# Optimization experiments

Hardware: AMD Instinct MI355X
Metric: run time of the kernel (lower is better)

## Reference

```python
import jax, jax.numpy as jnp
import numpy as np

EPS = 1e-8

def _normalize(x, eps=EPS):
    mean = jnp.mean(x, axis=-1, keepdims=True)
    var = jnp.var(x, axis=-1, keepdims=True)  # unbiased=False
    return (x - mean) / jnp.sqrt(var + eps)


def setup_inputs() -> dict:
    key = jax.random.key(0)
    ks = jax.random.split(key, 10)
    B, M, d = 8, 50000, 256
    out_units, num_heads, gsl_hidden = 256, 8, 16
    s = 0.02
    return {
        "h": jax.random.normal(ks[0], (B, M, d), dtype=jnp.float32),
        "att_w": jax.random.normal(ks[1], (d, num_heads), dtype=jnp.float32) * s,
        "att_b": jnp.zeros((num_heads,), dtype=jnp.float32),
        "w_w": jax.random.normal(ks[2], (d, out_units), dtype=jnp.float32) * s,
        "res_w": jax.random.normal(ks[3], (d, out_units), dtype=jnp.float32) * s,
        "res_b": jnp.zeros((out_units,), dtype=jnp.float32),
        "gsl1_w": jax.random.normal(ks[4], (d, gsl_hidden), dtype=jnp.float32) * s,
        "gsl1_b": jnp.zeros((gsl_hidden,), dtype=jnp.float32),
        "gsl2_w": jax.random.normal(ks[5], (gsl_hidden, 1), dtype=jnp.float32) * s,
        "gsl2_b": jnp.zeros((1,), dtype=jnp.float32),
        "k": 500,
    }


def reference(h, att_w, att_b, w_w, res_w, res_b, gsl1_w, gsl1_b, gsl2_w, gsl2_b, k):
    B, M, d = h.shape
    num_heads = att_w.shape[1]
    out_units = w_w.shape[1]
    head_dim = out_units // num_heads

    # additive attention scores per head: [B, M, H]
    A = jax.nn.relu(jnp.einsum('bmd,dh->bmh', h, att_w) + att_b)
    # value projection: [B, M, out]
    H_lin = jnp.einsum('bmd,de->bme', h, w_w)

    # learned graph-structure-learning scores: [B, M]
    S_hidden = jax.nn.relu(jnp.einsum('bmd,dg->bmg', h, gsl1_w) + gsl1_b)
    S = jax.nn.sigmoid(jnp.einsum('bmg,go->bmo', S_hidden, gsl2_w) + gsl2_b)[..., 0]

    # top-k mask over nodes (dim=1)
    k_eff = min(k, M)
    topk_vals, _ = jax.lax.top_k(S, k_eff)  # sorted descending
    kth = topk_vals[:, -1:]                 # [B, 1]
    mask = (S >= kth).astype(h.dtype)       # [B, M]

    # masked scores (zeros at masked positions, NOT -inf: faithful to source)
    A_mod = A * mask[:, :, None]            # [B, M, H]
    weights = jax.nn.softmax(A_mod, axis=1)  # softmax over M per head
    # (dropout is a no-op in eval mode)

    # per-head weighted sum over nodes, then concat heads along feature dim
    Hr = H_lin.reshape(B, M, num_heads, head_dim)
    out = jnp.einsum('bmh,bmhd->bhd', weights, Hr).reshape(B, 1, out_units)

    # residual from mean-pooled input
    Q_res = jax.nn.relu(jnp.einsum('bmd,de->bme', jnp.mean(h, axis=1, keepdims=True), res_w) + res_b)
    out = jax.nn.relu(out + Q_res)
    return _normalize(out), mask[:, None, :]
```

## Files before the change

kernel.cpp:

```cpp
#include <hip/hip_runtime.h>
#include <cstdint>
#include <cstddef>


#define MM     50000
#define BATCH  8
#define TILES  196
#define CH     8
#define NCHUNK 32

#define OFF_A        0u
#define OFF_KEYS     12800000u
#define OFF_SUMH     16000000u
#define OFF_UCORR    16016384u
#define OFF_ZCORR    16147456u
#define OFF_CCNT     16147968u
#define ZERO_SZ      148000u
#define OFF_KTH      16148000u
#define OFF_COMPACT  16148064u

__global__ __launch_bounds__(256) void k1_main(
    const float* __restrict__ h,
    const float* __restrict__ att_w,
    const float* __restrict__ att_b,
    const float* __restrict__ g1w,
    const float* __restrict__ g1b,
    const float* __restrict__ g2w,
    const float* __restrict__ g2b,
    float* __restrict__ Aout,
    unsigned long long* __restrict__ keys,
    double* __restrict__ sumh)
{
    __shared__ double gw_s[256][16];
    __shared__ float  aw_s[256][8];
    __shared__ float  tile[4][CH][65];
    __shared__ float  lsum[256];

    const int tid  = threadIdx.x;
    const int w    = tid >> 6;
    const int lane = tid & 63;

    for (int i = tid; i < 4096; i += 256) gw_s[i >> 4][i & 15] = (double)g1w[i];
    for (int i = tid; i < 2048; i += 256) aw_s[i >> 3][i & 7]  = att_w[i];
    lsum[tid] = 0.0f;
    __syncthreads();

    const int bid = blockIdx.x;
    const int b   = bid / TILES;
    const int t0  = bid % TILES;
    const int wave_row0 = t0 * 256 + w * 64;
    const size_t bbase = (size_t)b * MM;

    const int kq   = lane & 1;
    const int rsub = lane >> 1;

    float  aacc[8];
    double gacc[16];
#pragma unroll
    for (int j = 0; j < 8; ++j) aacc[j] = 0.0f;
#pragma unroll
    for (int g = 0; g < 16; ++g) gacc[g] = 0.0;

    const int m0 = wave_row0 + rsub;
    const int m1 = wave_row0 + 32 + rsub;
    const size_t r0c = bbase + (size_t)((m0 < MM) ? m0 : (MM - 1));
    const size_t r1c = bbase + (size_t)((m1 < MM) ? m1 : (MM - 1));

    {
        float4 v0 = *(const float4*)(h + r0c * 256 + kq * 4);
        float4 v1 = *(const float4*)(h + r1c * 256 + kq * 4);
        if (m0 >= MM) { v0.x = v0.y = v0.z = v0.w = 0.f; }
        if (m1 >= MM) { v1.x = v1.y = v1.z = v1.w = 0.f; }
        tile[w][kq*4+0][rsub] = v0.x;  tile[w][kq*4+1][rsub] = v0.y;
        tile[w][kq*4+2][rsub] = v0.z;  tile[w][kq*4+3][rsub] = v0.w;
        tile[w][kq*4+0][32+rsub] = v1.x;  tile[w][kq*4+1][32+rsub] = v1.y;
        tile[w][kq*4+2][32+rsub] = v1.z;  tile[w][kq*4+3][32+rsub] = v1.w;
    }

    for (int c = 0; c < NCHUNK; ++c) {
        float4 n0, n1;
        const bool has = (c + 1 < NCHUNK);
        if (has) {
            const int kof = (c + 1) * CH + kq * 4;
            n0 = *(const float4*)(h + r0c * 256 + kof);
            n1 = *(const float4*)(h + r1c * 256 + kof);
            if (m0 >= MM) { n0.x = n0.y = n0.z = n0.w = 0.f; }
            if (m1 >= MM) { n1.x = n1.y = n1.z = n1.w = 0.f; }
        }
        const int k0 = c * CH;
#pragma unroll
        for (int kk = 0; kk < CH; ++kk) {
            float  hv = tile[w][kk][lane];
            double hd = (double)hv;
            const int kx = k0 + kk;
#pragma unroll
            for (int j = 0; j < 8; ++j) aacc[j] = fmaf(hv, aw_s[kx][j], aacc[j]);
#pragma unroll
            for (int g = 0; g < 16; ++g) gacc[g] = fma(hd, gw_s[kx][g], gacc[g]);
        }
        {
            const int dsub = lane & 7;
            const int rq   = lane >> 3;
            float s = 0.f;
#pragma unroll
            for (int i = 0; i < 8; ++i) s += tile[w][dsub][rq * 8 + i];
            s += __shfl_xor(s, 8, 64);
            s += __shfl_xor(s, 16, 64);
            s += __shfl_xor(s, 32, 64);
            if (lane < 8) atomicAdd(&lsum[k0 + lane], s);
        }
        if (has) {
            tile[w][kq*4+0][rsub] = n0.x;  tile[w][kq*4+1][rsub] = n0.y;
            tile[w][kq*4+2][rsub] = n0.z;  tile[w][kq*4+3][rsub] = n0.w;
            tile[w][kq*4+0][32+rsub] = n1.x;  tile[w][kq*4+1][32+rsub] = n1.y;
            tile[w][kq*4+2][32+rsub] = n1.z;  tile[w][kq*4+3][32+rsub] = n1.w;
        }
    }

    const int m = wave_row0 + lane;
    if (m < MM) {
        size_t row = bbase + (size_t)m;
        float4 A0, A1;
        A0.x = fmaxf(aacc[0] + att_b[0], 0.f);
        A0.y = fmaxf(aacc[1] + att_b[1], 0.f);
        A0.z = fmaxf(aacc[2] + att_b[2], 0.f);
        A0.w = fmaxf(aacc[3] + att_b[3], 0.f);
        A1.x = fmaxf(aacc[4] + att_b[4], 0.f);
        A1.y = fmaxf(aacc[5] + att_b[5], 0.f);
        A1.z = fmaxf(aacc[6] + att_b[6], 0.f);
        A1.w = fmaxf(aacc[7] + att_b[7], 0.f);
        float4* Ap = (float4*)(Aout + row * 8);
        Ap[0] = A0; Ap[1] = A1;

        double z = (double)g2b[0];
#pragma unroll
        for (int g = 0; g < 16; ++g) {
            double sg = gacc[g] + (double)g1b[g];
            sg = sg > 0.0 ? sg : 0.0;
            z = fma(sg, (double)g2w[g], z);
        }
        long long uz = __double_as_longlong(z);
        unsigned long long key = (uz < 0)
            ? ~((unsigned long long)uz)
            : ((unsigned long long)uz | 0x8000000000000000ULL);
        keys[row] = key;
    }
    __syncthreads();
    atomicAdd(&sumh[b * 256 + tid], (double)lsum[tid]);
}

__global__ __launch_bounds__(1024) void k2_select(
    const unsigned long long* __restrict__ keys,
    const int* __restrict__ kptr,
    unsigned long long* __restrict__ kth)
{
    __shared__ unsigned long long buf[4096];
    __shared__ int s_cnt;
    __shared__ unsigned long long s_pivot;

    const int b    = blockIdx.x;
    const int tid  = threadIdx.x;
    const int lane = tid & 63;
    const size_t base = (size_t)b * MM;
    const int kval = min(*kptr, MM);

    buf[tid] = keys[base + (size_t)tid * 48];
    __syncthreads();
    for (int sz = 2; sz <= 1024; sz <<= 1)
        for (int j = sz >> 1; j > 0; j >>= 1) {
            __syncthreads();
            int i = tid, ixj = i ^ j;
            if (ixj > i) {
                unsigned long long a = buf[i], c = buf[ixj];
                bool up = ((i & sz) == 0);
                if ((up && a > c) || (!up && a < c)) { buf[i] = c; buf[ixj] = a; }
            }
        }
    __syncthreads();

    int R = 40;
    unsigned long long pivot = 0;
    for (int iter = 0; iter < 24; ++iter) {
        if (tid == 0) { s_pivot = buf[1023 - R]; s_cnt = 0; }
        __syncthreads();
        pivot = s_pivot;
        int loc = 0;
        for (int m = tid; m < MM; m += 1024)
            loc += (keys[base + m] >= pivot) ? 1 : 0;
        loc += __shfl_xor(loc, 32, 64);
        loc += __shfl_xor(loc, 16, 64);
        loc += __shfl_xor(loc, 8, 64);
        loc += __shfl_xor(loc, 4, 64);
        loc += __shfl_xor(loc, 2, 64);
        loc += __shfl_xor(loc, 1, 64);
        if (lane == 0) atomicAdd(&s_cnt, loc);
        __syncthreads();
        int n_ge = s_cnt;
        if (n_ge >= kval && n_ge <= 4096) break;
        R = (n_ge < kval) ? min(R + 48, 1023) : max(R - 16, 0);
        __syncthreads();
    }

    if (tid == 0) s_cnt = 0;
    __syncthreads();
    for (int m = tid; m < MM; m += 1024) {
        unsigned long long x = keys[base + m];
        bool p = (x >= pivot);
        unsigned long long ball = __ballot(p);
        int wbase = 0;
        if (lane == 0) { int wc = __popcll(ball); if (wc) wbase = atomicAdd(&s_cnt, wc); }
        wbase = __shfl(wbase, 0, 64);
        if (p) {
            int pos = wbase + __popcll(ball & ((1ull << lane) - 1ull));
            if (pos < 4096) buf[pos] = x;
        }
    }
    __syncthreads();
    const int n = min(s_cnt, 4096);

    unsigned long long p64 = 0;
    int kk = kval;
    for (int bit = 63; bit >= 0; --bit) {
        if (tid == 0) s_cnt = 0;
        __syncthreads();
        unsigned long long himask = (bit == 63) ? 0ull : (~0ull << (bit + 1));
        int loc = 0;
        for (int i = tid; i < n; i += 1024) {
            unsigned long long x = buf[i];
            if (((x ^ p64) & himask) == 0ull && ((x >> bit) & 1ull)) loc++;
        }
        loc += __shfl_xor(loc, 32, 64);
        loc += __shfl_xor(loc, 16, 64);
        loc += __shfl_xor(loc, 8, 64);
        loc += __shfl_xor(loc, 4, 64);
        loc += __shfl_xor(loc, 2, 64);
        loc += __shfl_xor(loc, 1, 64);
        if (lane == 0 && loc) atomicAdd(&s_cnt, loc);
        __syncthreads();
        int c1 = s_cnt;
        if (c1 >= kk) p64 |= (1ull << bit); else kk -= c1;
        __syncthreads();
    }
    if (tid == 0) kth[b] = p64;
}

__global__ __launch_bounds__(256) void k3_mask(
    const unsigned long long* __restrict__ keys,
    const unsigned long long* __restrict__ kth,
    float* __restrict__ maskout,
    int* __restrict__ ccnt,
    int* __restrict__ compact)
{
    int bid = blockIdx.x;
    int b = bid / TILES, t0 = bid % TILES;
    int m = t0 * 256 + threadIdx.x;
    int lane = threadIdx.x & 63;
    bool mk = false;
    if (m < MM) {
        size_t row = (size_t)b * MM + m;
        mk = (keys[row] >= kth[b]);
        maskout[row] = mk ? 1.0f : 0.0f;
    }
    unsigned long long ball = __ballot(mk);
    int wbase = 0;
    if (lane == 0) { int wc = __popcll(ball); if (wc) wbase = atomicAdd(&ccnt[b], wc); }
    wbase = __shfl(wbase, 0, 64);
    if (mk) {
        int pos = wbase + __popcll(ball & ((1ull << lane) - 1ull));
        if (pos < 2048) compact[b * 2048 + pos] = m;
    }
}

__global__ __launch_bounds__(256) void k4_corr(
    const float* __restrict__ h,
    const float* __restrict__ A,
    const int* __restrict__ compact,
    const int* __restrict__ ccnt,
    double* __restrict__ Ucorr,
    double* __restrict__ Zcorr)
{
    int b    = blockIdx.x >> 5;
    int part = blockIdx.x & 31;
    int tid  = threadIdx.x;
    int n = min(ccnt[b], 2048);
    float acc[8], zac[8];
#pragma unroll
    for (int j = 0; j < 8; ++j) { acc[j] = 0.f; zac[j] = 0.f; }
    for (int i = part; i < n; i += 32) {
        int m = compact[b * 2048 + i];
        size_t row = (size_t)b * MM + m;
        const float* Ap = A + row * 8;
        float hv = h[row * 256 + tid];
#pragma unroll
        for (int j = 0; j < 8; ++j) {
            float ex = expf(Ap[j]) - 1.0f;
            acc[j] = fmaf(ex, hv, acc[j]);
            zac[j] += ex;
        }
    }
#pragma unroll
    for (int j = 0; j < 8; ++j)
        atomicAdd(&Ucorr[(b * 8 + j) * 256 + tid], (double)acc[j]);
    if (tid == 0) {
#pragma unroll
        for (int j = 0; j < 8; ++j) atomicAdd(&Zcorr[b * 8 + j], (double)zac[j]);
    }
}

__global__ __launch_bounds__(256) void k5_final(
    const double* __restrict__ sumh,
    const double* __restrict__ Ucorr,
    const double* __restrict__ Zcorr,
    const int* __restrict__ ccnt,
    const float* __restrict__ w_w,
    const float* __restrict__ res_w,
    const float* __restrict__ res_b,
    float* __restrict__ out0)
{
    __shared__ float Us[8 * 256];
    __shared__ float ms[256];
    __shared__ float red[256];
    __shared__ float s_mean, s_var;

    int b = blockIdx.x, e = threadIdx.x;
    double sh = sumh[b * 256 + e];
    ms[e] = (float)sh;
#pragma unroll
    for (int j = 0; j < 8; ++j)
        Us[j * 256 + e] = (float)(sh + Ucorr[(b * 8 + j) * 256 + e]);
    __syncthreads();

    int hh = e >> 5;
    float Z = (float)((double)(MM - ccnt[b]) + Zcorr[b * 8 + hh]);
    float attn = 0.f, qr = 0.f;
    for (int d = 0; d < 256; ++d) {
        attn = fmaf(Us[hh * 256 + d], w_w[d * 256 + e], attn);
        qr   = fmaf(ms[d],            res_w[d * 256 + e], qr);
    }
    float qres = fmaxf(qr * (1.0f / (float)MM) + res_b[e], 0.f);
    float pre  = fmaxf(attn / Z + qres, 0.f);

    red[e] = pre; __syncthreads();
    for (int s = 128; s > 0; s >>= 1) { if (e < s) red[e] += red[e + s]; __syncthreads(); }
    if (e == 0) s_mean = red[0] * (1.0f / 256.0f);
    __syncthreads();
    float mean = s_mean;
    float dv = pre - mean;
    red[e] = dv * dv; __syncthreads();
    for (int s = 128; s > 0; s >>= 1) { if (e < s) red[e] += red[e + s]; __syncthreads(); }
    if (e == 0) s_var = red[0] * (1.0f / 256.0f);
    __syncthreads();
    out0[b * 256 + e] = dv / sqrtf(s_var + 1e-8f);
}

extern "C" void kernel_launch(void* const* d_in, const int* in_sizes, int n_in,
                              void* d_out, int out_size, void* d_ws, size_t ws_size,
                              hipStream_t stream) {
    const float* h     = (const float*)d_in[0];
    const float* att_w = (const float*)d_in[1];
    const float* att_b = (const float*)d_in[2];
    const float* w_w   = (const float*)d_in[3];
    const float* res_w = (const float*)d_in[4];
    const float* res_b = (const float*)d_in[5];
    const float* g1w   = (const float*)d_in[6];
    const float* g1b   = (const float*)d_in[7];
    const float* g2w   = (const float*)d_in[8];
    const float* g2b   = (const float*)d_in[9];
    const int*   kptr  = (const int*)d_in[10];

    char* ws = (char*)d_ws;
    float*              A       = (float*)(ws + OFF_A);
    unsigned long long* keys    = (unsigned long long*)(ws + OFF_KEYS);
    double*             sumh    = (double*)(ws + OFF_SUMH);
    double*             Ucorr   = (double*)(ws + OFF_UCORR);
    double*             Zcorr   = (double*)(ws + OFF_ZCORR);
    int*                ccnt    = (int*)(ws + OFF_CCNT);
    unsigned long long* kth     = (unsigned long long*)(ws + OFF_KTH);
    int*                compact = (int*)(ws + OFF_COMPACT);

    float* out0    = (float*)d_out;
    float* maskout = out0 + BATCH * 256;

    hipMemsetAsync(ws + OFF_SUMH, 0, ZERO_SZ, stream);

    k1_main  <<<BATCH*TILES, 256,  0, stream>>>(h, att_w, att_b, g1w, g1b, g2w, g2b,
                                                A, keys, sumh);
    k2_select<<<BATCH,       1024, 0, stream>>>(keys, kptr, kth);
    k3_mask  <<<BATCH*TILES, 256,  0, stream>>>(keys, kth, maskout, ccnt, compact);
    k4_corr  <<<BATCH*32,    256,  0, stream>>>(h, A, compact, ccnt, Ucorr, Zcorr);
    k5_final <<<BATCH,       256,  0, stream>>>(sumh, Ucorr, Zcorr, ccnt,
                                                w_w, res_w, res_b, out0);
}
```

Baseline: 937.1 us.

## Compute scores in fp32, refine top-k band candidates in fp64, recompute attention lazily

Result: faster. 830.1 us (-11.4%).

```diff
diff --git a/kernel.cpp b/kernel.cpp
--- a/kernel.cpp
+++ b/kernel.cpp
@@ -8,40 +8,43 @@
 #define TILES  196
 #define CH     8
 #define NCHUNK 32
-
-#define OFF_A        0u
-#define OFF_KEYS     12800000u
-#define OFF_SUMH     16000000u
-#define OFF_UCORR    16016384u
-#define OFF_ZCORR    16147456u
-#define OFF_CCNT     16147968u
-#define ZERO_SZ      148000u
-#define OFF_KTH      16148000u
-#define OFF_COMPACT  16148064u
+#define CANDCAP 4096
+#define COMPCAP 2048
+
+#define OFF_Z      0u
+#define OFF_CANDR  1600000u
+#define OFF_CANDK  1731072u
+#define OFF_COMP   1993216u
+#define OFF_LO     2058752u
+#define OFF_PAD    2058784u
+#define OFF_SUMH   2058848u
+#define OFF_UCORR  2075232u
+#define OFF_ZCORR  2206304u
+#define OFF_CCNT   2206816u
+#define OFF_CANDC  2206848u
+#define ZERO_OFF   OFF_SUMH
+#define ZERO_SZ    148032u
+
+__device__ __forceinline__ unsigned int f32_sortable(float z) {
+    unsigned int u = __float_as_uint(z);
+    return (u & 0x80000000u) ? ~u : (u | 0x80000000u);
+}
 
 __global__ __launch_bounds__(256) void k1_main(
     const float* __restrict__ h,
-    const float* __restrict__ att_w,
-    const float* __restrict__ att_b,
     const float* __restrict__ g1w,
     const float* __restrict__ g1b,
     const float* __restrict__ g2w,
     const float* __restrict__ g2b,
-    float* __restrict__ Aout,
-    unsigned long long* __restrict__ keys,
+    float* __restrict__ z32,
     double* __restrict__ sumh)
 {
-    __shared__ double gw_s[256][16];
-    __shared__ float  aw_s[256][8];
-    __shared__ float  tile[4][CH][65];
-    __shared__ float  lsum[256];
+    __shared__ float tile[4][CH][65];
+    __shared__ float lsum[256];
 
     const int tid  = threadIdx.x;
     const int w    = tid >> 6;
     const int lane = tid & 63;
-
-    for (int i = tid; i < 4096; i += 256) gw_s[i >> 4][i & 15] = (double)g1w[i];
-    for (int i = tid; i < 2048; i += 256) aw_s[i >> 3][i & 7]  = att_w[i];
     lsum[tid] = 0.0f;
     __syncthreads();
 
@@ -54,12 +57,9 @@
     const int kq   = lane & 1;
     const int rsub = lane >> 1;
 
-    float  aacc[8];
-    double gacc[16];
-#pragma unroll
-    for (int j = 0; j < 8; ++j) aacc[j] = 0.0f;
-#pragma unroll
-    for (int g = 0; g < 16; ++g) gacc[g] = 0.0;
+    float gacc[16];
+#pragma unroll
+    for (int g = 0; g < 16; ++g) gacc[g] = 0.0f;
 
     const int m0 = wave_row0 + rsub;
     const int m1 = wave_row0 + 32 + rsub;
@@ -90,13 +90,10 @@
         const int k0 = c * CH;
 #pragma unroll
         for (int kk = 0; kk < CH; ++kk) {
-            float  hv = tile[w][kk][lane];
-            double hd = (double)hv;
-            const int kx = k0 + kk;
-#pragma unroll
-            for (int j = 0; j < 8; ++j) aacc[j] = fmaf(hv, aw_s[kx][j], aacc[j]);
-#pragma unroll
-            for (int g = 0; g < 16; ++g) gacc[g] = fma(hd, gw_s[kx][g], gacc[g]);
+            float hv = tile[w][kk][lane];
+            const float* gw = g1w + (k0 + kk) * 16;
+#pragma unroll
+            for (int g = 0; g < 16; ++g) gacc[g] = fmaf(hv, gw[g], gacc[g]);
         }
         {
             const int dsub = lane & 7;
@@ -119,104 +116,145 @@
 
     const int m = wave_row0 + lane;
     if (m < MM) {
-        size_t row = bbase + (size_t)m;
-        float4 A0, A1;
-        A0.x = fmaxf(aacc[0] + att_b[0], 0.f);
-        A0.y = fmaxf(aacc[1] + att_b[1], 0.f);
-        A0.z = fmaxf(aacc[2] + att_b[2], 0.f);
-        A0.w = fmaxf(aacc[3] + att_b[3], 0.f);
-        A1.x = fmaxf(aacc[4] + att_b[4], 0.f);
-        A1.y = fmaxf(aacc[5] + att_b[5], 0.f);
-        A1.z = fmaxf(aacc[6] + att_b[6], 0.f);
-        A1.w = fmaxf(aacc[7] + att_b[7], 0.f);
-        float4* Ap = (float4*)(Aout + row * 8);
-        Ap[0] = A0; Ap[1] = A1;
-
-        double z = (double)g2b[0];
+        float z = g2b[0];
 #pragma unroll
         for (int g = 0; g < 16; ++g) {
-            double sg = gacc[g] + (double)g1b[g];
-            sg = sg > 0.0 ? sg : 0.0;
-            z = fma(sg, (double)g2w[g], z);
-        }
-        long long uz = __double_as_longlong(z);
-        unsigned long long key = (uz < 0)
-            ? ~((unsigned long long)uz)
-            : ((unsigned long long)uz | 0x8000000000000000ULL);
-        keys[row] = key;
+            float sg = gacc[g] + g1b[g];
+            sg = fmaxf(sg, 0.0f);
+            z = fmaf(sg, g2w[g], z);
+        }
+        z32[bbase + m] = z;
     }
     __syncthreads();
     atomicAdd(&sumh[b * 256 + tid], (double)lsum[tid]);
 }
 
-__global__ __launch_bounds__(1024) void k2_select(
-    const unsigned long long* __restrict__ keys,
+__global__ __launch_bounds__(1024) void k2_sample(
+    const float* __restrict__ z32,
     const int* __restrict__ kptr,
-    unsigned long long* __restrict__ kth)
-{
-    __shared__ unsigned long long buf[4096];
-    __shared__ int s_cnt;
-    __shared__ unsigned long long s_pivot;
-
-    const int b    = blockIdx.x;
-    const int tid  = threadIdx.x;
-    const int lane = tid & 63;
+    unsigned int* __restrict__ lo_out)
+{
+    __shared__ unsigned int buf[1024];
+    const int b   = blockIdx.x;
+    const int tid = threadIdx.x;
     const size_t base = (size_t)b * MM;
     const int kval = min(*kptr, MM);
 
-    buf[tid] = keys[base + (size_t)tid * 48];
+    int idx = (int)(((long long)tid * MM) / 1024);
+    buf[tid] = f32_sortable(z32[base + idx]);
     __syncthreads();
     for (int sz = 2; sz <= 1024; sz <<= 1)
         for (int j = sz >> 1; j > 0; j >>= 1) {
             __syncthreads();
             int i = tid, ixj = i ^ j;
             if (ixj > i) {
-                unsigned long long a = buf[i], c = buf[ixj];
+                unsigned int a = buf[i], c = buf[ixj];
                 bool up = ((i & sz) == 0);
                 if ((up && a > c) || (!up && a < c)) { buf[i] = c; buf[ixj] = a; }
             }
         }
     __syncthreads();
-
-    int R = 40;
-    unsigned long long pivot = 0;
-    for (int iter = 0; iter < 24; ++iter) {
-        if (tid == 0) { s_pivot = buf[1023 - R]; s_cnt = 0; }
-        __syncthreads();
-        pivot = s_pivot;
-        int loc = 0;
-        for (int m = tid; m < MM; m += 1024)
-            loc += (keys[base + m] >= pivot) ? 1 : 0;
-        loc += __shfl_xor(loc, 32, 64);
-        loc += __shfl_xor(loc, 16, 64);
-        loc += __shfl_xor(loc, 8, 64);
-        loc += __shfl_xor(loc, 4, 64);
-        loc += __shfl_xor(loc, 2, 64);
-        loc += __shfl_xor(loc, 1, 64);
-        if (lane == 0) atomicAdd(&s_cnt, loc);
-        __syncthreads();
-        int n_ge = s_cnt;
-        if (n_ge >= kval && n_ge <= 4096) break;
-        R = (n_ge < kval) ? min(R + 48, 1023) : max(R - 16, 0);
-        __syncthreads();
-    }
-
-    if (tid == 0) s_cnt = 0;
-    __syncthreads();
-    for (int m = tid; m < MM; m += 1024) {
-        unsigned long long x = keys[base + m];
-        bool p = (x >= pivot);
-        unsigned long long ball = __ballot(p);
-        int wbase = 0;
-        if (lane == 0) { int wc = __popcll(ball); if (wc) wbase = atomicAdd(&s_cnt, wc); }
-        wbase = __shfl(wbase, 0, 64);
-        if (p) {
-            int pos = wbase + __popcll(ball & ((1ull << lane) - 1ull));
-            if (pos < 4096) buf[pos] = x;
-        }
-    }
-    __syncthreads();
-    const int n = min(s_cnt, 4096);
+    if (tid == 0) {
+        int ks = (int)(((long long)kval * 1024) / MM) + 35;
+        ks = min(1023, max(1, ks));
+        lo_out[b] = buf[1023 - ks];
+    }
+}
+
+__global__ __launch_bounds__(256) void k3_band(
+    const float* __restrict__ z32,
+    const unsigned int* __restrict__ lo_in,
+    float* __restrict__ maskout,
+    int* __restrict__ cand_cnt,
+    int* __restrict__ cand_rows)
+{
+    int bid = blockIdx.x;
+    int b = bid / TILES, t0 = bid % TILES;
+    int m = t0 * 256 + threadIdx.x;
+    int lane = threadIdx.x & 63;
+    bool cand = false;
+    if (m < MM) {
+        size_t row = (size_t)b * MM + m;
+        cand = (f32_sortable(z32[row]) >= lo_in[b]);
+        if (!cand) maskout[row] = 0.0f;
+    }
+    unsigned long long ball = __ballot(cand);
+    int wbase = 0;
+    if (lane == 0) { int wc = __popcll(ball); if (wc) wbase = atomicAdd(&cand_cnt[b], wc); }
+    wbase = __shfl(wbase, 0, 64);
+    if (cand) {
+        int pos = wbase + __popcll(ball & ((1ull << lane) - 1ull));
+        if (pos < CANDCAP) cand_rows[b * CANDCAP + pos] = m;
+    }
+}
+
+__global__ __launch_bounds__(256) void k3r_refine(
+    const float* __restrict__ h,
+    const float* __restrict__ g1w,
+    const float* __restrict__ g1b,
+    const float* __restrict__ g2w,
+    const float* __restrict__ g2b,
+    const int* __restrict__ cand_cnt,
+    const int* __restrict__ cand_rows,
+    unsigned long long* __restrict__ cand_keys)
+{
+    __shared__ double g1s[256][16];
+    const int b    = blockIdx.x >> 4;
+    const int part = blockIdx.x & 15;
+    const int tid  = threadIdx.x;
+    for (int i = tid; i < 4096; i += 256) g1s[i >> 4][i & 15] = (double)g1w[i];
+    __syncthreads();
+
+    const int n = min(cand_cnt[b], CANDCAP);
+    const size_t bbase = (size_t)b * MM;
+    for (int slot = part * 256 + tid; slot < n; slot += 4096) {
+        int row = cand_rows[b * CANDCAP + slot];
+        const float* hp = h + (bbase + (size_t)row) * 256;
+        double gacc[16];
+#pragma unroll
+        for (int g = 0; g < 16; ++g) gacc[g] = 0.0;
+        for (int k = 0; k < 256; ++k) {
+            double hd = (double)hp[k];
+#pragma unroll
+            for (int g = 0; g < 16; ++g) gacc[g] = fma(hd, g1s[k][g], gacc[g]);
+        }
+        double z = (double)g2b[0];
+#pragma unroll
+        for (int g = 0; g < 16; ++g) {
+            double sg = gacc[g] + (double)g1b[g];
+            sg = sg > 0.0 ? sg : 0.0;
+            z = fma(sg, (double)g2w[g], z);
+        }
+        long long uz = __double_as_longlong(z);
+        unsigned long long key = (uz < 0)
+            ? ~((unsigned long long)uz)
+            : ((unsigned long long)uz | 0x8000000000000000ULL);
+        cand_keys[b * CANDCAP + slot] = key;
+    }
+}
+
+__global__ __launch_bounds__(1024) void k3s_select(
+    const int* __restrict__ kptr,
+    const int* __restrict__ cand_cnt,
+    const int* __restrict__ cand_rows,
+    const unsigned long long* __restrict__ cand_keys,
+    float* __restrict__ maskout,
+    int* __restrict__ ccnt,
+    int* __restrict__ compact)
+{
+    __shared__ unsigned long long kbuf[CANDCAP];
+    __shared__ int s_cnt;
+
+    const int b    = blockIdx.x;
+    const int tid  = threadIdx.x;
+    const int lane = tid & 63;
+    const int n = min(cand_cnt[b], CANDCAP);
+    const size_t bbase = (size_t)b * MM;
+    int kval = min(*kptr, MM);
+    if (kval > n) kval = n;
+
+    for (int i = tid; i < n; i += 1024) kbuf[i] = cand_keys[b * CANDCAP + i];
+    __syncthreads();
 
     unsigned long long p64 = 0;
     int kk = kval;
@@ -226,7 +264,7 @@
         unsigned long long himask = (bit == 63) ? 0ull : (~0ull << (bit + 1));
         int loc = 0;
         for (int i = tid; i < n; i += 1024) {
-            unsigned long long x = buf[i];
+            unsigned long long x = kbuf[i];
             if (((x ^ p64) & himask) == 0ull && ((x >> bit) & 1ull)) loc++;
         }
         loc += __shfl_xor(loc, 32, 64);
@@ -241,62 +279,75 @@
         if (c1 >= kk) p64 |= (1ull << bit); else kk -= c1;
         __syncthreads();
     }
-    if (tid == 0) kth[b] = p64;
-}
-
-__global__ __launch_bounds__(256) void k3_mask(
-    const unsigned long long* __restrict__ keys,
-    const unsigned long long* __restrict__ kth,
-    float* __restrict__ maskout,
-    int* __restrict__ ccnt,
-    int* __restrict__ compact)
-{
-    int bid = blockIdx.x;
-    int b = bid / TILES, t0 = bid % TILES;
-    int m = t0 * 256 + threadIdx.x;
-    int lane = threadIdx.x & 63;
-    bool mk = false;
-    if (m < MM) {
-        size_t row = (size_t)b * MM + m;
-        mk = (keys[row] >= kth[b]);
-        maskout[row] = mk ? 1.0f : 0.0f;
-    }
-    unsigned long long ball = __ballot(mk);
-    int wbase = 0;
-    if (lane == 0) { int wc = __popcll(ball); if (wc) wbase = atomicAdd(&ccnt[b], wc); }
-    wbase = __shfl(wbase, 0, 64);
-    if (mk) {
-        int pos = wbase + __popcll(ball & ((1ull << lane) - 1ull));
-        if (pos < 2048) compact[b * 2048 + pos] = m;
+
+    for (int i0 = 0; i0 < n; i0 += 1024) {
+        int i = i0 + tid;
+        bool active = (i < n);
+        bool mk = false;
+        int row = 0;
+        if (active) {
+            row = cand_rows[b * CANDCAP + i];
+            mk = (kbuf[i] >= p64);
+            maskout[bbase + row] = mk ? 1.0f : 0.0f;
+        }
+        unsigned long long ball = __ballot(mk);
+        int wbase = 0;
+        if (lane == 0) { int wc = __popcll(ball); if (wc) wbase = atomicAdd(&ccnt[b], wc); }
+        wbase = __shfl(wbase, 0, 64);
+        if (mk) {
+            int pos = wbase + __popcll(ball & ((1ull << lane) - 1ull));
+            if (pos < COMPCAP) compact[b * COMPCAP + pos] = row;
+        }
     }
 }
 
 __global__ __launch_bounds__(256) void k4_corr(
     const float* __restrict__ h,
-    const float* __restrict__ A,
+    const float* __restrict__ att_w,
+    const float* __restrict__ att_b,
     const int* __restrict__ compact,
     const int* __restrict__ ccnt,
     double* __restrict__ Ucorr,
     double* __restrict__ Zcorr)
 {
-    int b    = blockIdx.x >> 5;
-    int part = blockIdx.x & 31;
-    int tid  = threadIdx.x;
-    int n = min(ccnt[b], 2048);
+    __shared__ float hv_s[256];
+    __shared__ float a_s[8];
+
+    const int b    = blockIdx.x >> 5;
+    const int part = blockIdx.x & 31;
+    const int tid  = threadIdx.x;
+    const int head = tid >> 5;
+    const int seg  = tid & 31;
+    const size_t bbase = (size_t)b * MM;
+    const int n = min(ccnt[b], COMPCAP);
+
     float acc[8], zac[8];
 #pragma unroll
     for (int j = 0; j < 8; ++j) { acc[j] = 0.f; zac[j] = 0.f; }
+
     for (int i = part; i < n; i += 32) {
-        int m = compact[b * 2048 + i];
-        size_t row = (size_t)b * MM + m;
-        const float* Ap = A + row * 8;
-        float hv = h[row * 256 + tid];
+        int row = compact[b * COMPCAP + i];
+        float hv = h[(bbase + (size_t)row) * 256 + tid];
+        hv_s[tid] = hv;
+        __syncthreads();
+        float p = 0.f;
+#pragma unroll
+        for (int j = 0; j < 8; ++j)
+            p = fmaf(hv_s[seg * 8 + j], att_w[(seg * 8 + j) * 8 + head], p);
+        p += __shfl_xor(p, 1, 64);
+        p += __shfl_xor(p, 2, 64);
+        p += __shfl_xor(p, 4, 64);
+        p += __shfl_xor(p, 8, 64);
+        p += __shfl_xor(p, 16, 64);
+        if (seg == 0) a_s[head] = fmaxf(p + att_b[head], 0.f);
+        __syncthreads();
 #pragma unroll
         for (int j = 0; j < 8; ++j) {
-            float ex = expf(Ap[j]) - 1.0f;
-            acc[j] = fmaf(ex, hv, acc[j]);
-            zac[j] += ex;
-        }
+            float w8 = expf(a_s[j]) - 1.0f;
+            acc[j] = fmaf(w8, hv, acc[j]);
+            zac[j] += w8;
+        }
+        __syncthreads();
     }
 #pragma unroll
     for (int j = 0; j < 8; ++j)
@@ -369,25 +420,31 @@
     const int*   kptr  = (const int*)d_in[10];
 
     char* ws = (char*)d_ws;
-    float*              A       = (float*)(ws + OFF_A);
-    unsigned long long* keys    = (unsigned long long*)(ws + OFF_KEYS);
+    float*              z32     = (float*)(ws + OFF_Z);
+    int*                candr   = (int*)(ws + OFF_CANDR);
+    unsigned long long* candk   = (unsigned long long*)(ws + OFF_CANDK);
+    int*                compact = (int*)(ws + OFF_COMP);
+    unsigned int*       lo      = (unsigned int*)(ws + OFF_LO);
     double*             sumh    = (double*)(ws + OFF_SUMH);
     double*             Ucorr   = (double*)(ws + OFF_UCORR);
     double*             Zcorr   = (double*)(ws + OFF_ZCORR);
     int*                ccnt    = (int*)(ws + OFF_CCNT);
-    unsigned long long* kth     = (unsigned long long*)(ws + OFF_KTH);
-    int*                compact = (int*)(ws + OFF_COMPACT);
+    int*                candc   = (int*)(ws + OFF_CANDC);
 
     float* out0    = (float*)d_out;
     float* maskout = out0 + BATCH * 256;
 
-    hipMemsetAsync(ws + OFF_SUMH, 0, ZERO_SZ, stream);
-
-    k1_main  <<<BATCH*TILES, 256,  0, stream>>>(h, att_w, att_b, g1w, g1b, g2w, g2b,
-                                                A, keys, sumh);
-    k2_select<<<BATCH,       1024, 0, stream>>>(keys, kptr, kth);
-    k3_mask  <<<BATCH*TILES, 256,  0, stream>>>(keys, kth, maskout, ccnt, compact);
-    k4_corr  <<<BATCH*32,    256,  0, stream>>>(h, A, compact, ccnt, Ucorr, Zcorr);
-    k5_final <<<BATCH,       256,  0, stream>>>(sumh, Ucorr, Zcorr, ccnt,
-                                                w_w, res_w, res_b, out0);
-}
+    hipMemsetAsync(ws + ZERO_OFF, 0, ZERO_SZ, stream);
+
+    k1_main   <<<BATCH*TILES, 256,  0, stream>>>(h, g1w, g1b, g2w, g2b, z32, sumh);
+    k2_sample <<<BATCH,       1024, 0, stream>>>(z32, kptr, lo);
+    k3_band   <<<BATCH*TILES, 256,  0, stream>>>(z32, lo, maskout, candc, candr);
+    k3r_refine<<<BATCH*16,    256,  0, stream>>>(h, g1w, g1b, g2w, g2b,
+                                                 candc, candr, candk);
+    k3s_select<<<BATCH,       1024, 0, stream>>>(kptr, candc, candr, candk,
+                                                 maskout, ccnt, compact);
+    k4_corr   <<<BATCH*32,    256,  0, stream>>>(h, att_w, att_b, compact, ccnt,
+                                                 Ucorr, Zcorr);
+    k5_final  <<<BATCH,       256,  0, stream>>>(sumh, Ucorr, Zcorr, ccnt,
+                                                 w_w, res_w, res_b, out0);
+}
```
